# Optimization experiments

Hardware: AMD Instinct MI355X
Metric: run time of the kernel (lower is better)

Reference implementation:

```python
import jax, jax.numpy as jnp
import numpy as np

N, T = 8192, 2048

def setup_inputs() -> dict:
    key = jax.random.key(0)
    k1, k2, k3 = jax.random.split(key, 3)
    # sorted event times via cumsum of small inter-event gaps (max total ~10.24)
    dt = jax.random.uniform(k1, (N, T), dtype=jnp.float32) * 0.005
    event_times = jnp.cumsum(dt, axis=1)
    input_mask = (jax.random.uniform(k2, (N, T)) < 0.9).astype(jnp.float32)
    spatial_locations = jax.random.normal(k3, (N, T, 2), dtype=jnp.float32)
    t0 = jnp.zeros((1,), dtype=jnp.float32)
    t1 = jnp.full((1,), 11.0, dtype=jnp.float32)  # > max event time
    mu_param = jnp.array([-2.0], dtype=jnp.float32)   # matches randn*0.5-2.0 init scale
    beta_param = jnp.array([0.0], dtype=jnp.float32)  # matches randn*0.5 init scale
    return {"event_times": event_times, "spatial_locations": spatial_locations,
            "input_mask": input_mask, "t0": t0, "t1": t1,
            "mu_param": mu_param, "beta_param": beta_param}

def reference(event_times, spatial_locations, input_mask, t0, t1, mu_param, beta_param):
    del spatial_locations  # unused, as in the torch module
    n, t = event_times.shape
    mu = jax.nn.softplus(mu_param)[0]
    beta = jax.nn.softplus(beta_param)[0]

    # log-likelihood term: sum_i mask_i * (mu*t_i - beta*i)
    betaN = beta * jnp.arange(t, dtype=event_times.dtype)  # (T,)
    loglik = ((mu * event_times - betaN) * input_mask).sum(-1)  # (N,)

    # Recurrence vectorized: N_i = exclusive cumsum of mask; t0_i = forward-fill
    # of masked event times, seeded with t0. Terms where mask==0 are exactly 0
    # in the original loop (t1_i == t0_i), so we multiply by the mask.
    mask_b = input_mask > 0.5
    cN = jnp.cumsum(input_mask, axis=1)           # inclusive count (N,T)
    exclN = cN - input_mask                        # N_i before step i
    pos = jnp.where(mask_b, jnp.arange(1, t + 1, dtype=jnp.int32), 0)  # (N,T)
    idx_incl = jax.lax.cummax(pos, axis=1)         # index (1-based) of last masked event up to i
    idx_excl = jnp.concatenate([jnp.zeros((n, 1), dtype=idx_incl.dtype), idx_incl[:, :-1]], axis=1)
    t0_b = jnp.broadcast_to(t0.reshape(-1), (n,))
    t1_b = jnp.broadcast_to(t1.reshape(-1), (n,))
    vals = jnp.concatenate([t0_b[:, None], event_times], axis=1)  # (N, T+1), index 0 -> t0
    prev_t = jnp.take_along_axis(vals, idx_excl, axis=1)           # t0_i at step i
    last_t = jnp.take_along_axis(vals, idx_incl[:, -1:], axis=1)[:, 0]  # final t0_i

    terms = input_mask * jnp.exp(-beta * exclN) / mu * (jnp.exp(mu * event_times) - jnp.exp(mu * prev_t))
    compensator = terms.sum(-1) + jnp.exp(-beta * cN[:, -1]) / mu * (jnp.exp(mu * t1_b) - jnp.exp(mu * last_t))
    return loglik - compensator
```

## Files before the change

### kernel.cpp

```cpp
#include <hip/hip_runtime.h>
#include <math.h>


#define T_LEN 2048
#define CHUNK 256

__global__ __launch_bounds__(256) void scpp_kernel(
    const float* __restrict__ event_times,
    const float* __restrict__ input_mask,
    const float* __restrict__ t0p, const float* __restrict__ t1p,
    const float* __restrict__ mup, const float* __restrict__ betap,
    float* __restrict__ out, int n_rows)
{
    const int lane = threadIdx.x & 63;
    const int row  = blockIdx.x * 4 + (threadIdx.x >> 6);
    if (row >= n_rows) return;

    const float t0   = t0p[0];
    const float t1   = t1p[0];
    const float mu   = log1pf(expf(mup[0]));
    const float beta = log1pf(expf(betap[0]));

    const float* tr = event_times + (size_t)row * T_LEN;
    const float* mr = input_mask  + (size_t)row * T_LEN;

    const float NEG = -3.402823466e38f;
    float carry_cnt  = 0.f;
    float carry_maxt = t0;
    float ll = 0.f, comp = 0.f;

    #pragma unroll
    for (int c = 0; c < T_LEN / CHUNK; ++c) {
        const int base = c * CHUNK + lane * 4;
        const float4 tv = *(const float4*)(tr + base);
        const float4 mv = *(const float4*)(mr + base);
        float t[4] = {tv.x, tv.y, tv.z, tv.w};
        float m[4] = {mv.x, mv.y, mv.z, mv.w};

        float cnt_ex[4], mt_ex[4];
        float acc_cnt = 0.f, acc_mt = NEG;
        #pragma unroll
        for (int j = 0; j < 4; ++j) {
            cnt_ex[j] = acc_cnt;
            mt_ex[j]  = acc_mt;
            acc_cnt += m[j];
            acc_mt   = fmaxf(acc_mt, (m[j] > 0.5f) ? t[j] : NEG);
        }

        float inc_cnt = acc_cnt, inc_mt = acc_mt;
        #pragma unroll
        for (int d = 1; d < 64; d <<= 1) {
            float vc = __shfl_up(inc_cnt, d, 64);
            float vm = __shfl_up(inc_mt,  d, 64);
            if (lane >= d) { inc_cnt += vc; inc_mt = fmaxf(inc_mt, vm); }
        }
        float ex_cnt = inc_cnt - acc_cnt;
        float ex_mt  = __shfl_up(inc_mt, 1, 64);
        if (lane == 0) ex_mt = NEG;

        #pragma unroll
        for (int j = 0; j < 4; ++j) {
            const float exclN = carry_cnt + ex_cnt + cnt_ex[j];
            const float prevt = fmaxf(carry_maxt, fmaxf(ex_mt, mt_ex[j]));
            comp += m[j] * expf(-beta * exclN) *
                    (expf(mu * t[j]) - expf(mu * prevt));
            ll   += m[j] * (mu * t[j] - beta * (float)(base + j));
        }

        carry_cnt  += __shfl(inc_cnt, 63, 64);
        carry_maxt  = fmaxf(carry_maxt, __shfl(inc_mt, 63, 64));
    }

    #pragma unroll
    for (int d = 32; d >= 1; d >>= 1) {
        ll   += __shfl_xor(ll,   d, 64);
        comp += __shfl_xor(comp, d, 64);
    }

    if (lane == 0) {
        const float tail = expf(-beta * carry_cnt) *
                           (expf(mu * t1) - expf(mu * carry_maxt));
        out[row] = ll - (comp + tail) / mu;
    }
}

extern "C" void kernel_launch(void* const* d_in, const int* in_sizes, int n_in,
                              void* d_out, int out_size, void* d_ws, size_t ws_size,
                              hipStream_t stream) {
    const float* event_times = (const float*)d_in[0];
    const float* input_mask  = (const float*)d_in[2];
    const float* t0          = (const float*)d_in[3];
    const float* t1          = (const float*)d_in[4];
    const float* mu_param    = (const float*)d_in[5];
    const float* beta_param  = (const float*)d_in[6];
    float* out = (float*)d_out;

    const int n_rows = in_sizes[0] / T_LEN;
    dim3 grid((n_rows + 3) / 4);
    scpp_kernel<<<grid, 256, 0, stream>>>(event_times, input_mask, t0, t1,
                                          mu_param, beta_param, out, n_rows);
}
```

Baseline: 252.3 us.

## Telescope compensator sum and replace shuffle scans with ballot/mbcnt counts

Rewrites the compensator algebraically as a telescoping sum. Each masked event contributes exp(mu*t - beta*exclN), and the previous-event terms collapse to a (1-q) factor, so the forward-fill max-scan and the second exp per element are no longer needed. The exclusive mask count is computed with wavefront ballot plus mbcnt/popcount instead of a 6-step shuffle scan, and the log-likelihood is split into two plain accumulated sums. Fast __expf intrinsics replace expf, and the ballot path assumes the mask is exactly 0/1 (threshold vs. value), which may change numerics and precision.

Result: no change. 249.4 us (-1.1%).

```diff
diff --git a/kernel.cpp b/kernel.cpp
--- a/kernel.cpp
+++ b/kernel.cpp
@@ -24,63 +24,52 @@
     const float* tr = event_times + (size_t)row * T_LEN;
     const float* mr = input_mask  + (size_t)row * T_LEN;
 
-    const float NEG = -3.402823466e38f;
-    float carry_cnt  = 0.f;
-    float carry_maxt = t0;
-    float ll = 0.f, comp = 0.f;
+    float carry = 0.f;
+    float S = 0.f, S1 = 0.f, S2 = 0.f;
 
     #pragma unroll
     for (int c = 0; c < T_LEN / CHUNK; ++c) {
         const int base = c * CHUNK + lane * 4;
         const float4 tv = *(const float4*)(tr + base);
         const float4 mv = *(const float4*)(mr + base);
-        float t[4] = {tv.x, tv.y, tv.z, tv.w};
-        float m[4] = {mv.x, mv.y, mv.z, mv.w};
+        const float t[4] = {tv.x, tv.y, tv.z, tv.w};
+        const float m[4] = {mv.x, mv.y, mv.z, mv.w};
 
-        float cnt_ex[4], mt_ex[4];
-        float acc_cnt = 0.f, acc_mt = NEG;
+        unsigned below_i = 0, tot_i = 0;
         #pragma unroll
         for (int j = 0; j < 4; ++j) {
-            cnt_ex[j] = acc_cnt;
-            mt_ex[j]  = acc_mt;
-            acc_cnt += m[j];
-            acc_mt   = fmaxf(acc_mt, (m[j] > 0.5f) ? t[j] : NEG);
+            const unsigned long long b = __ballot(m[j] > 0.5f);
+            below_i += __builtin_amdgcn_mbcnt_hi((unsigned)(b >> 32),
+                       __builtin_amdgcn_mbcnt_lo((unsigned)b, 0u));
+            tot_i   += (unsigned)__popcll(b);
         }
+        const float below = (float)below_i;
 
-        float inc_cnt = acc_cnt, inc_mt = acc_mt;
-        #pragma unroll
-        for (int d = 1; d < 64; d <<= 1) {
-            float vc = __shfl_up(inc_cnt, d, 64);
-            float vm = __shfl_up(inc_mt,  d, 64);
-            if (lane >= d) { inc_cnt += vc; inc_mt = fmaxf(inc_mt, vm); }
-        }
-        float ex_cnt = inc_cnt - acc_cnt;
-        float ex_mt  = __shfl_up(inc_mt, 1, 64);
-        if (lane == 0) ex_mt = NEG;
-
+        float local = 0.f;
         #pragma unroll
         for (int j = 0; j < 4; ++j) {
-            const float exclN = carry_cnt + ex_cnt + cnt_ex[j];
-            const float prevt = fmaxf(carry_maxt, fmaxf(ex_mt, mt_ex[j]));
-            comp += m[j] * expf(-beta * exclN) *
-                    (expf(mu * t[j]) - expf(mu * prevt));
-            ll   += m[j] * (mu * t[j] - beta * (float)(base + j));
+            const float exclN = carry + below + local;
+            const float arg   = fmaf(mu, t[j], -beta * exclN);
+            S  = fmaf(m[j], __expf(arg), S);
+            S1 = fmaf(m[j], t[j], S1);
+            S2 = fmaf(m[j], (float)(base + j), S2);
+            local += m[j];
         }
-
-        carry_cnt  += __shfl(inc_cnt, 63, 64);
-        carry_maxt  = fmaxf(carry_maxt, __shfl(inc_mt, 63, 64));
+        carry += (float)tot_i;
     }
 
     #pragma unroll
     for (int d = 32; d >= 1; d >>= 1) {
-        ll   += __shfl_xor(ll,   d, 64);
-        comp += __shfl_xor(comp, d, 64);
+        S  += __shfl_xor(S,  d, 64);
+        S1 += __shfl_xor(S1, d, 64);
+        S2 += __shfl_xor(S2, d, 64);
     }
 
     if (lane == 0) {
-        const float tail = expf(-beta * carry_cnt) *
-                           (expf(mu * t1) - expf(mu * carry_maxt));
-        out[row] = ll - (comp + tail) / mu;
+        const float q   = __expf(-beta);
+        const float qK  = __expf(-beta * carry);
+        const float C   = (1.f - q) * S + qK * __expf(mu * t1) - __expf(mu * t0);
+        out[row] = (mu * S1 - beta * S2) - C / mu;
     }
 }
 
```
